# Kernel tuning notes

Measured on AMD Instinct MI355X. Metric: run time of the kernel, lower is better.

## Reference

```python
import jax, jax.numpy as jnp
import numpy as np


def setup_inputs() -> dict:
    key = jax.random.key(0)
    k1, k2 = jax.random.split(key)
    N, C, H, W = 4, 128, 160, 320
    left = jax.random.normal(k1, (N, C, H, W), dtype=jnp.float32)
    right = jax.random.normal(k2, (N, C, H, W), dtype=jnp.float32)
    return {"left": left, "right": right, "max_disparity": 48}


def reference(left, right, max_disparity):
    # left, right: (N, C, H, W) -> volume: (N, D, H, W)
    # volume[n, d, h, w] = sum_c left[n, c, h, w] * right[n, c, h, w - d]  (0 if w < d)
    n, c, h, w = left.shape
    slices = []
    for d in range(max_disparity):  # fixed structural constant, unrolled at trace time
        # channel dot-product of overlapping strips, shape (N, H, W - d)
        corr = jnp.einsum('nchw,nchw->nhw', left[:, :, :, d:], right[:, :, :, :w - d])
        # left-pad the first d columns with zeros to restore width W
        slices.append(jnp.pad(corr, ((0, 0), (0, 0), (d, 0))))
    return jnp.stack(slices, axis=1)  # (N, D, H, W)
```

## Files before the change

### kernel.cpp

```cpp
#include <hip/hip_runtime.h>
#include <stdint.h>


#define NN 4
#define CC 128
#define HH 160
#define WW 320
#define DD 48
#define HWs (HH * WW)
#define WB 160
#define RJ 208
#define CK 32
#define CHF (CK * RJ)
#define NTH 640
#define GRID 1280

typedef _Float16 h2 __attribute__((ext_vector_type(2)));
typedef _Float16 f16x8 __attribute__((ext_vector_type(8)));
typedef float f32x4 __attribute__((ext_vector_type(4)));
typedef __fp16 h2raw __attribute__((ext_vector_type(2)));

__device__ __forceinline__ h2 pack2(float a, float b) {
  union { h2raw r; h2 h; } u;
  u.r = __builtin_amdgcn_cvt_pkrtz(a, b);
  return u.h;
}

__device__ __forceinline__ void gl_lds16(const float* g, float* l) {
  __builtin_amdgcn_global_load_lds(
      (const __attribute__((address_space(1))) uint32_t*)g,
      (__attribute__((address_space(3))) uint32_t*)l, 16, 0, 0);
}

__global__ __launch_bounds__(NTH, 8)
void corr_kernel(const float* __restrict__ L, const float* __restrict__ R,
                 float* __restrict__ out) {
  __shared__ __align__(16) float S[2 * CHF];

  const int tid = threadIdx.x;
  const int wt  = tid >> 6;
  const int ln  = tid & 63;
  const int i16 = ln & 15;
  const int g   = ln >> 4;

  const int raw = blockIdx.x;
  const int bid = (raw & 7) * (GRID / 8) + (raw >> 3);
  const int wsplit = bid & 1;
  const int rnh = bid >> 1;
  const int n = rnh / HH;
  const int h = rnh - n * HH;
  const int wb = wsplit * WB;

  const size_t base = (size_t)n * CC * HWs + (size_t)h * WW;
  const float* Rb = R + base;
  const float* Lb = L + base + wb + 16 * wt + i16;

  const int t0 = tid, t1 = tid + 640, t2 = tid + 1280;
  const int c0 = t0 / 52, v0 = t0 - 52 * c0;
  const int c1 = t1 / 52, v1 = t1 - 52 * c1;
  const int c2 = t2 / 52, v2 = t2 - 52 * c2;
  int col0 = wb - 48 + 4 * v0; if (col0 < 0) col0 = 0;
  int col1 = wb - 48 + 4 * v1; if (col1 < 0) col1 = 0;
  int col2 = wb - 48 + 4 * v2; if (col2 < 0) col2 = 0;
  const float* gp0 = Rb + (size_t)c0 * HWs + col0;
  const float* gp1 = Rb + (size_t)c1 * HWs + col1;
  const float* gp2 = Rb + (size_t)c2 * HWs + col2;

  float lv[2][8];

  auto stage = [&](int kk) {
    float* dst = S + (kk & 1) * CHF;
    const size_t coff = (size_t)(CK * kk) * HWs;
    gl_lds16(gp0 + coff, dst + 4 * t0);
    gl_lds16(gp1 + coff, dst + 4 * t1);
    if (wt < 6) gl_lds16(gp2 + coff, dst + 4 * t2);
  };
  auto lload = [&](int kk) {
    const float* p = Lb + (size_t)(CK * kk) * HWs;
#pragma unroll
    for (int e = 0; e < 8; ++e)
      lv[kk & 1][e] = p[(size_t)(4 * e + g) * HWs];
  };

  stage(0);
  lload(0);
  __syncthreads();

  f32x4 acc[4];
#pragma unroll
  for (int q = 0; q < 4; ++q) acc[q] = (f32x4){0.f, 0.f, 0.f, 0.f};

#pragma unroll
  for (int k = 0; k < 4; ++k) {
    if (k < 3) { stage(k + 1); lload(k + 1); }

    union AU { f16x8 v; h2 h[4]; } A;
#pragma unroll
    for (int j = 0; j < 4; ++j)
      A.h[j] = pack2(lv[k & 1][2 * j], lv[k & 1][2 * j + 1]);

    const float* Bb = S + (k & 1) * CHF;
#pragma unroll
    for (int q = 0; q < 4; ++q) {
      const int s = 16 * (wt + q) + i16;
      union BU { f16x8 v; h2 h[4]; } B;
#pragma unroll
      for (int j = 0; j < 4; ++j)
        B.h[j] = pack2(Bb[(8 * j + g) * RJ + s], Bb[(8 * j + 4 + g) * RJ + s]);
      acc[q] = __builtin_amdgcn_mfma_f32_16x16x32_f16(A.v, B.v, acc[q], 0, 0, 0);
    }
    __syncthreads();
  }

  float* ep = S + wt * (DD * 20);
  const int wl = wb + 16 * wt;
#pragma unroll
  for (int q = 0; q < 4; ++q)
#pragma unroll
    for (int r = 0; r < 4; ++r) {
      const int m = 4 * g + r;
      const int d = 48 - 16 * q + m - i16;
      if (d >= 0 && d < DD) ep[d * 20 + m] = (d <= wl + m) ? acc[q][r] : 0.f;
    }

  const int l4 = ln & 3;
  const int dr = ln >> 2;
  float* op = out + (size_t)n * DD * HWs + (size_t)h * WW + wl + 4 * l4;
#pragma unroll
  for (int rr = 0; rr < 3; ++rr) {
    const int d = 16 * rr + dr;
    *(float4*)&op[(size_t)d * HWs] = *(const float4*)&ep[d * 20 + 4 * l4];
  }
}

extern "C" void kernel_launch(void* const* d_in, const int* in_sizes, int n_in,
                              void* d_out, int out_size, void* d_ws, size_t ws_size,
                              hipStream_t stream) {
  const float* L = (const float*)d_in[0];
  const float* R = (const float*)d_in[1];
  float* out = (float*)d_out;
  corr_kernel<<<dim3(GRID), dim3(NTH), 0, stream>>>(L, R, out);
}
```

Before: 245.1 us.

## Split each row into five 64-wide blocks with smaller channel chunks

Each block now covers one row and a 64-column strip instead of half a row. That gives 3200 blocks of 256 threads instead of 1280 blocks of 640. The channel loop moves to 16-channel chunks across 8 stages, and the MFMA changes from 16x16x32 to 16x16x16 f16. The goal is finer-grained parallelism and a smaller LDS footprint for higher occupancy. In exchange, the overlapping right-image halo (48 extra columns per 64 outputs) is loaded more often, and there are more barriers per block.

New measurement: 245.3 us. No clear change (+0.1%).

```diff
diff --git a/kernel.cpp b/kernel.cpp
--- a/kernel.cpp
+++ b/kernel.cpp
@@ -8,15 +8,15 @@
 #define WW 320
 #define DD 48
 #define HWs (HH * WW)
-#define WB 160
-#define RJ 208
-#define CK 32
-#define CHF (CK * RJ)
-#define NTH 640
-#define GRID 1280
+#define WQ 64
+#define WIN 116
+#define CK 16
+#define CHF (CK * WIN)
+#define NTH 256
+#define GRID 3200
 
+typedef _Float16 f16x4 __attribute__((ext_vector_type(4)));
 typedef _Float16 h2 __attribute__((ext_vector_type(2)));
-typedef _Float16 f16x8 __attribute__((ext_vector_type(8)));
 typedef float f32x4 __attribute__((ext_vector_type(4)));
 typedef __fp16 h2raw __attribute__((ext_vector_type(2)));
 
@@ -35,50 +35,49 @@
 __global__ __launch_bounds__(NTH, 8)
 void corr_kernel(const float* __restrict__ L, const float* __restrict__ R,
                  float* __restrict__ out) {
-  __shared__ __align__(16) float S[2 * CHF];
+  __shared__ __align__(16) float S[3840];
 
   const int tid = threadIdx.x;
-  const int wt  = tid >> 6;
+  const int wid = tid >> 6;
   const int ln  = tid & 63;
   const int i16 = ln & 15;
   const int g   = ln >> 4;
 
   const int raw = blockIdx.x;
   const int bid = (raw & 7) * (GRID / 8) + (raw >> 3);
-  const int wsplit = bid & 1;
-  const int rnh = bid >> 1;
+
+  const int rnh = bid / 5;
+  const int wq  = bid - 5 * rnh;
   const int n = rnh / HH;
   const int h = rnh - n * HH;
-  const int wb = wsplit * WB;
+  const int wb = wq * WQ;
 
   const size_t base = (size_t)n * CC * HWs + (size_t)h * WW;
   const float* Rb = R + base;
-  const float* Lb = L + base + wb + 16 * wt + i16;
+  const float* Lb = L + base + wb + 16 * wid + i16;
 
-  const int t0 = tid, t1 = tid + 640, t2 = tid + 1280;
-  const int c0 = t0 / 52, v0 = t0 - 52 * c0;
-  const int c1 = t1 / 52, v1 = t1 - 52 * c1;
-  const int c2 = t2 / 52, v2 = t2 - 52 * c2;
-  int col0 = wb - 48 + 4 * v0; if (col0 < 0) col0 = 0;
-  int col1 = wb - 48 + 4 * v1; if (col1 < 0) col1 = 0;
-  int col2 = wb - 48 + 4 * v2; if (col2 < 0) col2 = 0;
+  const int t0 = tid, t1 = tid + NTH;
+  const int c0 = t0 / 29, v0 = t0 - 29 * c0;
+  const int c1 = t1 / 29, v1 = t1 - 29 * c1;
+  int col0 = wb - 48 + 4 * v0;
+  int col1 = wb - 48 + 4 * v1;
+  if (col0 < 0) col0 = 0; if (col0 > WW - 4) col0 = WW - 4;
+  if (col1 < 0) col1 = 0; if (col1 > WW - 4) col1 = WW - 4;
   const float* gp0 = Rb + (size_t)c0 * HWs + col0;
   const float* gp1 = Rb + (size_t)c1 * HWs + col1;
-  const float* gp2 = Rb + (size_t)c2 * HWs + col2;
 
-  float lv[2][8];
+  float lv[2][4];
 
   auto stage = [&](int kk) {
     float* dst = S + (kk & 1) * CHF;
     const size_t coff = (size_t)(CK * kk) * HWs;
     gl_lds16(gp0 + coff, dst + 4 * t0);
-    gl_lds16(gp1 + coff, dst + 4 * t1);
-    if (wt < 6) gl_lds16(gp2 + coff, dst + 4 * t2);
+    if (t1 < 464) gl_lds16(gp1 + coff, dst + 4 * t1);
   };
   auto lload = [&](int kk) {
     const float* p = Lb + (size_t)(CK * kk) * HWs;
 #pragma unroll
-    for (int e = 0; e < 8; ++e)
+    for (int e = 0; e < 4; ++e)
       lv[kk & 1][e] = p[(size_t)(4 * e + g) * HWs];
   };
 
@@ -91,29 +90,27 @@
   for (int q = 0; q < 4; ++q) acc[q] = (f32x4){0.f, 0.f, 0.f, 0.f};
 
 #pragma unroll
-  for (int k = 0; k < 4; ++k) {
-    if (k < 3) { stage(k + 1); lload(k + 1); }
+  for (int k = 0; k < 8; ++k) {
+    if (k < 7) { stage(k + 1); lload(k + 1); }
 
-    union AU { f16x8 v; h2 h[4]; } A;
-#pragma unroll
-    for (int j = 0; j < 4; ++j)
-      A.h[j] = pack2(lv[k & 1][2 * j], lv[k & 1][2 * j + 1]);
+    union AU { f16x4 v; h2 h[2]; } A;
+    A.h[0] = pack2(lv[k & 1][0], lv[k & 1][1]);
+    A.h[1] = pack2(lv[k & 1][2], lv[k & 1][3]);
 
     const float* Bb = S + (k & 1) * CHF;
 #pragma unroll
     for (int q = 0; q < 4; ++q) {
-      const int s = 16 * (wt + q) + i16;
-      union BU { f16x8 v; h2 h[4]; } B;
-#pragma unroll
-      for (int j = 0; j < 4; ++j)
-        B.h[j] = pack2(Bb[(8 * j + g) * RJ + s], Bb[(8 * j + 4 + g) * RJ + s]);
-      acc[q] = __builtin_amdgcn_mfma_f32_16x16x32_f16(A.v, B.v, acc[q], 0, 0, 0);
+      const int s = 16 * (wid + q) + i16;
+      union BU { f16x4 v; h2 h[2]; } B;
+      B.h[0] = pack2(Bb[(g) * WIN + s], Bb[(4 + g) * WIN + s]);
+      B.h[1] = pack2(Bb[(8 + g) * WIN + s], Bb[(12 + g) * WIN + s]);
+      acc[q] = __builtin_amdgcn_mfma_f32_16x16x16f16(A.v, B.v, acc[q], 0, 0, 0);
     }
     __syncthreads();
   }
 
-  float* ep = S + wt * (DD * 20);
-  const int wl = wb + 16 * wt;
+  float* ep = S + wid * (DD * 20);
+  const int wl = wb + 16 * wid;
 #pragma unroll
   for (int q = 0; q < 4; ++q)
 #pragma unroll
```
